# Optimization experiments

Hardware: AMD Instinct MI355X
Metric: run time of the kernel (lower is better)

Reference implementation:

```python
import jax, jax.numpy as jnp
import numpy as np

ALPHA = 0.2  # LeakyReLU negative slope
NEG_BIG = -9e15


def setup_inputs() -> dict:
    key = jax.random.key(0)
    k1, k2, k3, k4 = jax.random.split(key, 4)
    B, N, F_in, F_out = 8, 2048, 256, 256
    x = jax.random.normal(k1, (B, N, F_in), dtype=jnp.float32)
    adj = jax.random.randint(k2, (B, N, N), 0, 2, dtype=jnp.int32)
    # Xavier-uniform init like nn.init.xavier_uniform_
    limW = float(np.sqrt(6.0 / (F_in + F_out)))
    W = jax.random.uniform(k3, (F_in, F_out), minval=-limW, maxval=limW, dtype=jnp.float32)
    lima = float(np.sqrt(6.0 / (2 * F_out + 1)))
    a = jax.random.uniform(k4, (2 * F_out, 1), minval=-lima, maxval=lima, dtype=jnp.float32)
    return {"x": x, "adj": adj, "W": W, "a": a}


def reference(x, adj, W, a):
    # x: (B,N,Fin), adj: (B,N,N), W: (Fin,Fout), a: (2*Fout,1)
    F_out = W.shape[1]
    Wh = jnp.einsum('bnf,fo->bno', x, W)            # (B,N,Fout)
    a1, a2 = a[:F_out, 0], a[F_out:, 0]
    # e[b,i,j] = leakyrelu(Wh[b,i]@a1 + Wh[b,j]@a2)  (equivalent to concat+matmul)
    e = (Wh @ a1)[:, :, None] + (Wh @ a2)[:, None, :]  # (B,N,N)
    e = jnp.where(e > 0, e, ALPHA * e)
    attention = jnp.where(adj > 0, e, NEG_BIG)
    attention = jax.nn.softmax(attention, axis=-1)
    # dropout is identity in eval mode (training=False)
    h_prime = jnp.einsum('bij,bjo->bio', attention, Wh)  # (B,N,Fout)
    return jax.nn.elu(h_prime)  # concat=True -> ELU
```

## Files before the change

kernel.cpp:

```cpp
#include <hip/hip_runtime.h>
#include <hip/hip_fp16.h>

typedef _Float16 f16;
typedef _Float16 half4 __attribute__((ext_vector_type(4)));
typedef _Float16 half8 __attribute__((ext_vector_type(8)));
typedef float f32x4 __attribute__((ext_vector_type(4)));

#define BATCH 8
#define NTOK 2048
#define FIN 256
#define FOUT 256
#define ALPHA 0.2f


__device__ __forceinline__ void gload16(const void* g, void* l) {
    __builtin_amdgcn_global_load_lds(
        (const __attribute__((address_space(1))) unsigned int*)(g),
        (__attribute__((address_space(3))) unsigned int*)(l), 16, 0, 0);
}

__global__ void k_wt(const float* __restrict__ W, f16* __restrict__ WT) {
    __shared__ float t[32][33];
    int o0 = blockIdx.x * 32, k0 = blockIdx.y * 32;
    int tx = threadIdx.x, ty = threadIdx.y;
    t[ty][tx] = W[(k0 + ty) * FOUT + o0 + tx];
    __syncthreads();
    WT[(o0 + ty) * FIN + (k0 + tx)] = (f16)t[tx][ty];
}

__global__ __launch_bounds__(256) void k_gemm(const float* __restrict__ x,
                                              const f16* __restrict__ WT,
                                              const float* __restrict__ a,
                                              f16* __restrict__ WhT,
                                              float* __restrict__ s1,
                                              float* __restrict__ s2) {
    __shared__ __align__(16) char gsmem[46080];
    int t = threadIdx.x;
    int lane = t & 63, w = t >> 6;
    f16* Ah = (f16*)gsmem;
    f16* Bt = (f16*)(gsmem + 9216);
    int m0 = blockIdx.x * 64;
    int lr = lane & 15, lg = lane >> 4;
    f32x4 acc[4][4] = {};

    for (int k0 = 0; k0 < FIN; k0 += 64) {
        {
            int r = t >> 2, c = (t & 3) * 16;
            const float* src = x + (size_t)(m0 + r) * FIN + k0 + c;
            f32x4 v0 = *(const f32x4*)(src);
            f32x4 v1 = *(const f32x4*)(src + 4);
            f32x4 v2 = *(const f32x4*)(src + 8);
            f32x4 v3 = *(const f32x4*)(src + 12);
            half8 h0, h1;
#pragma unroll
            for (int q = 0; q < 4; q++) {
                h0[q] = (f16)v0[q]; h0[q + 4] = (f16)v1[q];
                h1[q] = (f16)v2[q]; h1[q + 4] = (f16)v3[q];
            }
            f16* dst = Ah + r * 72 + c;
            *(half8*)dst = h0;
            *(half8*)(dst + 8) = h1;
        }
        {
            const f16* src = WT + (size_t)t * FIN + k0;
            f16* dst = Bt + t * 72;
#pragma unroll
            for (int q = 0; q < 8; q++)
                *(half8*)(dst + q * 8) = *(const half8*)(src + q * 8);
        }
        __syncthreads();
#pragma unroll
        for (int kc = 0; kc < 2; kc++) {
            int krow = kc * 32 + lg * 8;
            half8 af[4], bf[4];
#pragma unroll
            for (int fi = 0; fi < 4; fi++)
                af[fi] = *(half8*)(Ah + (fi * 16 + lr) * 72 + krow);
#pragma unroll
            for (int fo = 0; fo < 4; fo++)
                bf[fo] = *(half8*)(Bt + (w * 64 + fo * 16 + lr) * 72 + krow);
#pragma unroll
            for (int fi = 0; fi < 4; fi++)
#pragma unroll
                for (int fo = 0; fo < 4; fo++)
                    acc[fi][fo] = __builtin_amdgcn_mfma_f32_16x16x32_f16(
                        af[fi], bf[fo], acc[fi][fo], 0, 0, 0);
        }
        __syncthreads();
    }

    int b = m0 >> 11;
    int slab_i = (m0 & (NTOK - 1)) >> 6;
    int nbase = m0 & (NTOK - 1);

    float* sred = (float*)gsmem;
    f16* slab = (f16*)(gsmem + 9216);
    float a1v[4], a2v[4];
#pragma unroll
    for (int fo = 0; fo < 4; fo++) {
        int o = w * 64 + fo * 16 + lr;
        a1v[fo] = a[o];
        a2v[fo] = a[FOUT + o];
    }
#pragma unroll
    for (int fi = 0; fi < 4; fi++) {
        f32x4 p1 = {}, p2 = {};
#pragma unroll
        for (int fo = 0; fo < 4; fo++) {
            p1 += acc[fi][fo] * a1v[fo];
            p2 += acc[fi][fo] * a2v[fo];
        }
#pragma unroll
        for (int q = 0; q < 4; q++) {
#pragma unroll
            for (int d = 1; d < 16; d <<= 1) {
                p1[q] += __shfl_xor(p1[q], d);
                p2[q] += __shfl_xor(p2[q], d);
            }
        }
        if (lr == 0) {
            int row = fi * 16 + lg * 4;
#pragma unroll
            for (int q = 0; q < 4; q++) {
                sred[w * 64 + row + q] = p1[q];
                sred[256 + w * 64 + row + q] = p2[q];
            }
        }
    }
#pragma unroll
    for (int fi = 0; fi < 4; fi++) {
        int jg8 = fi * 2 + (lg >> 1), jq0 = (lg & 1) * 4;
#pragma unroll
        for (int fo = 0; fo < 4; fo++) {
            int o = w * 64 + fo * 16 + lr;
            half4 hv;
#pragma unroll
            for (int q = 0; q < 4; q++) hv[q] = (f16)acc[fi][fo][q];
            *(half4*)(slab + o * 64 + ((jg8 ^ (o & 7)) * 8) + jq0) = hv;
        }
    }
    __syncthreads();

    if (t < 64) {
        s1[(size_t)b * NTOK + nbase + t] =
            sred[t] + sred[64 + t] + sred[128 + t] + sred[192 + t];
    } else if (t < 128) {
        int r2 = t - 64;
        s2[(size_t)b * NTOK + nbase + r2] =
            sred[256 + r2] + sred[320 + r2] + sred[384 + r2] + sred[448 + r2];
    }
    {
        const int4* sl = (const int4*)slab;
        int4* gd = (int4*)(WhT + ((size_t)(b * 32 + slab_i) * 256) * 64);
#pragma unroll
        for (int i = 0; i < 8; i++) gd[i * 256 + t] = sl[i * 256 + t];
    }
}

__global__ __launch_bounds__(512, 1) void k_attn(const int* __restrict__ adj,
                                                 const f16* __restrict__ WhT,
                                                 const float* __restrict__ s1g,
                                                 const float* __restrict__ s2g,
                                                 float* __restrict__ out) {
    __shared__ __align__(16) char smem[91264];
    f16* Bl = (f16*)smem;
    float* s2_lds = (float*)(smem + 65536);
    unsigned* mask_lds = (unsigned*)(smem + 73728);
    float* lpart = (float*)(smem + 90624);
    float* wmax = (float*)(smem + 91136);

    int b = blockIdx.x & 7;
    int i0 = (blockIdx.x >> 3) * 64;
    int t = threadIdx.x;
    int lane = t & 63, w = t >> 6;
    int js = w & 1, oh = (w >> 1) & 1, rg = w >> 2;
    int lr = lane & 15, lg = lane >> 4;

    {
        f32x4 sv4 = ((const f32x4*)(s2g + (size_t)b * NTOK))[t];
        ((f32x4*)s2_lds)[t] = sv4;
        float tmx = fmaxf(fmaxf(sv4[0], sv4[1]), fmaxf(sv4[2], sv4[3]));
#pragma unroll
        for (int d = 1; d < 64; d <<= 1) tmx = fmaxf(tmx, __shfl_xor(tmx, d));
        if (lane == 0) wmax[w] = tmx;
    }

    const char* wsrc = (const char*)WhT + (size_t)b * (32 * 32768);
    {
        const char* src = wsrc + (w * 4) * 1024 + lane * 16;
        char* dst = (char*)Bl + (w * 4) * 1024;
#pragma unroll
        for (int k = 0; k < 4; k++) gload16(src + k * 1024, dst + k * 1024);
    }

    {
        const int4* abase = (const int4*)(adj + ((size_t)(b * NTOK + i0 + w * 8)) * NTOK)
                            + lane * 8;
        int4 cur[8], nxt[8];
#pragma unroll
        for (int k = 0; k < 8; k++) cur[k] = abase[k];
        for (int r = 0; r < 8; r++) {
            if (r < 7) {
#pragma unroll
                for (int k = 0; k < 8; k++) nxt[k] = abase[(r + 1) * 512 + k];
            }
            unsigned m = 0;
#pragma unroll
            for (int k = 0; k < 8; k++) {
                m |= (unsigned)(cur[k].x > 0) << (k * 4);
                m |= (unsigned)(cur[k].y > 0) << (k * 4 + 1);
                m |= (unsigned)(cur[k].z > 0) << (k * 4 + 2);
                m |= (unsigned)(cur[k].w > 0) << (k * 4 + 3);
            }
            mask_lds[(w * 8 + r) * 66 + lane] = m;
#pragma unroll
            for (int k = 0; k < 8; k++) cur[k] = nxt[k];
        }
    }

    int rr0 = rg * 32 + lr;
    int r0 = i0 + rr0, r1 = r0 + 16;
    float s1r0 = s1g[(size_t)b * NTOK + r0];
    float s1r1 = s1g[(size_t)b * NTOK + r1];

    f32x4 acc0[8] = {}, acc1[8] = {};
    float l0 = 0.f, l1 = 0.f;
    int rswz = ((js * 4 + lg) ^ (lr & 7)) * 8;

    __syncthreads();

    float s2m = wmax[0];
#pragma unroll
    for (int k = 1; k < 8; k++) s2m = fmaxf(s2m, wmax[k]);
    float tx0 = s1r0 + s2m;
    float mx0 = fmaxf(tx0, ALPHA * tx0);
    float tx1 = s1r1 + s2m;
    float mx1 = fmaxf(tx1, ALPHA * tx1);

    for (int s = 0; s < 32; s++) {
        int buf = s & 1;
        if (s < 31) {
            const char* src = wsrc + (size_t)(s + 1) * 32768 + (w * 4) * 1024 + lane * 16;
            char* dst = (char*)Bl + (buf ^ 1) * 32768 + (w * 4) * 1024;
#pragma unroll
            for (int k = 0; k < 4; k++) gload16(src + k * 1024, dst + k * 1024);
        }

        unsigned cw0 = mask_lds[rr0 * 66 + s * 2 + js];
        unsigned cw1 = mask_lds[(rr0 + 16) * 66 + s * 2 + js];
        unsigned bits0 = (cw0 >> (lg * 8)) & 0xffu;
        unsigned bits1 = (cw1 >> (lg * 8)) & 0xffu;

        int sb = s * 64 + js * 32 + lg * 8;
        f32x4 sA = *(const f32x4*)&s2_lds[sb];
        f32x4 sB = *(const f32x4*)&s2_lds[sb + 4];

        half8 ph0, ph1;
#pragma unroll
        for (int q = 0; q < 8; q++) {
            float sv = q < 4 ? sA[q & 3] : sB[q & 3];
            float sx = s1r0 + sv;
            float ev = fmaxf(sx, ALPHA * sx);
            float p = ((bits0 >> q) & 1) ? __expf(ev - mx0) : 0.f;
            l0 += p; ph0[q] = (f16)p;
            float sy = s1r1 + sv;
            float eu = fmaxf(sy, ALPHA * sy);
            float u = ((bits1 >> q) & 1) ? __expf(eu - mx1) : 0.f;
            l1 += u; ph1[q] = (f16)u;
        }

        const f16* bbase = Bl + buf * 16384 + (oh * 128 + lr) * 64 + rswz;
#pragma unroll
        for (int ot = 0; ot < 8; ot++) {
            half8 bf = *(const half8*)(bbase + ot * (16 * 64));
            acc0[ot] = __builtin_amdgcn_mfma_f32_16x16x32_f16(ph0, bf, acc0[ot], 0, 0, 0);
            acc1[ot] = __builtin_amdgcn_mfma_f32_16x16x32_f16(ph1, bf, acc1[ot], 0, 0, 0);
        }
        __syncthreads();
    }

    l0 += __shfl_xor(l0, 16); l0 += __shfl_xor(l0, 32);
    l1 += __shfl_xor(l1, 16); l1 += __shfl_xor(l1, 32);
    if (oh == 0 && lg == 0) {
        lpart[js * 64 + rg * 32 + lr] = l0;
        lpart[js * 64 + rg * 32 + 16 + lr] = l1;
    }
    __syncthreads();

    float* accx = (float*)smem;
    if (js == 1) {
#pragma unroll
        for (int ot = 0; ot < 8; ot++)
#pragma unroll
            for (int q = 0; q < 4; q++) {
                accx[(rg * 32 + lg * 4 + q) * 260 + oh * 128 + ot * 16 + lr] = acc0[ot][q];
                accx[(rg * 32 + 16 + lg * 4 + q) * 260 + oh * 128 + ot * 16 + lr] = acc1[ot][q];
            }
    }
    __syncthreads();
    if (js == 0) {
        f32x4 rl0, rl1;
#pragma unroll
        for (int q = 0; q < 4; q++) {
            int ra = rg * 32 + lg * 4 + q, rb = ra + 16;
            rl0[q] = 1.f / (lpart[ra] + lpart[64 + ra]);
            rl1[q] = 1.f / (lpart[rb] + lpart[64 + rb]);
        }
#pragma unroll
        for (int ot = 0; ot < 8; ot++) {
            int o = oh * 128 + ot * 16 + lr;
#pragma unroll
            for (int q = 0; q < 4; q++) {
                int ra = rg * 32 + lg * 4 + q;
                float u = (acc0[ot][q] + accx[ra * 260 + o]) * rl0[q];
                u = u > 0.f ? u : __expf(u) - 1.f;
                __builtin_nontemporal_store(u, &out[((size_t)(b * NTOK + i0 + ra)) * FOUT + o]);
                int rb = ra + 16;
                float v = (acc1[ot][q] + accx[rb * 260 + o]) * rl1[q];
                v = v > 0.f ? v : __expf(v) - 1.f;
                __builtin_nontemporal_store(v, &out[((size_t)(b * NTOK + i0 + rb)) * FOUT + o]);
            }
        }
    }
}

extern "C" void kernel_launch(void* const* d_in, const int* in_sizes, int n_in,
                              void* d_out, int out_size, void* d_ws, size_t ws_size,
                              hipStream_t stream) {
    const float* x = (const float*)d_in[0];
    const int* adj = (const int*)d_in[1];
    const float* W = (const float*)d_in[2];
    const float* a = (const float*)d_in[3];
    float* out = (float*)d_out;

    char* ws = (char*)d_ws;
    f16* WT = (f16*)ws;
    f16* WhT = (f16*)(ws + 131072);
    float* s1 = (float*)(ws + 131072 + 8388608);
    float* s2 = s1 + BATCH * NTOK;

    k_wt<<<dim3(FOUT / 32, FIN / 32), dim3(32, 32), 0, stream>>>(W, WT);
    k_gemm<<<dim3(BATCH * NTOK / 64), 256, 0, stream>>>(x, WT, a, WhT, s1, s2);
    k_attn<<<dim3(BATCH * NTOK / 64), 512, 0, stream>>>(adj, WhT, s1, s2, out);
}
```

Baseline: 82.85 us.

## Compute softmax probabilities once into LDS and split MFMA work by output columns

Before, each warp pair split the key dimension, so every warp recomputed exp for 32 rows across half the keys, and the two halves were reduced through LDS at the end. Now each thread computes the probabilities for one row and eight keys exactly once per step and writes them as f16 into a swizzled LDS tile. All warps then read A fragments from that tile and each covers a quarter of the output columns, which removes the redundant exp work and the final cross-warp reduction. The change also folds log2e into s1/s2 so exp2f can be used, and issues the WhT prefetch two stages ahead. The cost is a second barrier per step, extra LDS traffic for P, and a larger LDS footprint.

```diff
diff --git a/kernel.cpp b/kernel.cpp
--- a/kernel.cpp
+++ b/kernel.cpp
@@ -11,6 +11,7 @@
 #define FIN 256
 #define FOUT 256
 #define ALPHA 0.2f
+#define LOG2E 1.44269504088896340736f
 
 
 __device__ __forceinline__ void gload16(const void* g, void* l) {
@@ -162,22 +163,26 @@
                                                  const float* __restrict__ s1g,
                                                  const float* __restrict__ s2g,
                                                  float* __restrict__ out) {
-    __shared__ __align__(16) char smem[91264];
+    __shared__ __align__(16) char smem[107296];
     f16* Bl = (f16*)smem;
     float* s2_lds = (float*)(smem + 65536);
     unsigned* mask_lds = (unsigned*)(smem + 73728);
-    float* lpart = (float*)(smem + 90624);
-    float* wmax = (float*)(smem + 91136);
+    f16* P_lds = (f16*)(smem + 90624);
+    float* l_lds = (float*)(smem + 107008);
+    float* wmax = (float*)(smem + 107264);
 
     int b = blockIdx.x & 7;
     int i0 = (blockIdx.x >> 3) * 64;
     int t = threadIdx.x;
     int lane = t & 63, w = t >> 6;
-    int js = w & 1, oh = (w >> 1) & 1, rg = w >> 2;
     int lr = lane & 15, lg = lane >> 4;
+    int oq = w & 3, rg = w >> 2;
+    int r4 = lane >> 3, j8 = lane & 7;
+    int srow = w * 8 + r4;
 
     {
         f32x4 sv4 = ((const f32x4*)(s2g + (size_t)b * NTOK))[t];
+        sv4 = sv4 * LOG2E;
         ((f32x4*)s2_lds)[t] = sv4;
         float tmx = fmaxf(fmaxf(sv4[0], sv4[1]), fmaxf(sv4[2], sv4[3]));
 #pragma unroll
@@ -187,139 +192,141 @@
 
     const char* wsrc = (const char*)WhT + (size_t)b * (32 * 32768);
     {
-        const char* src = wsrc + (w * 4) * 1024 + lane * 16;
-        char* dst = (char*)Bl + (w * 4) * 1024;
-#pragma unroll
-        for (int k = 0; k < 4; k++) gload16(src + k * 1024, dst + k * 1024);
+        const char* s0 = wsrc + w * 4096 + lane * 16;
+        char* d0 = (char*)Bl + w * 4096;
+#pragma unroll
+        for (int k = 0; k < 4; k++) gload16(s0 + k * 1024, d0 + k * 1024);
+        const char* s1p = wsrc + 32768 + w * 4096 + lane * 16;
+        char* d1 = (char*)Bl + 32768 + w * 4096;
+#pragma unroll
+        for (int k = 0; k < 4; k++) gload16(s1p + k * 1024, d1 + k * 1024);
     }
 
     {
         const int4* abase = (const int4*)(adj + ((size_t)(b * NTOK + i0 + w * 8)) * NTOK)
                             + lane * 8;
-        int4 cur[8], nxt[8];
-#pragma unroll
-        for (int k = 0; k < 8; k++) cur[k] = abase[k];
-        for (int r = 0; r < 8; r++) {
-            if (r < 7) {
-#pragma unroll
-                for (int k = 0; k < 8; k++) nxt[k] = abase[(r + 1) * 512 + k];
-            }
-            unsigned m = 0;
+        int4 c0[8], c1[8];
+#pragma unroll
+        for (int k = 0; k < 8; k++) { c0[k] = abase[k]; c1[k] = abase[512 + k]; }
+        for (int rp = 0; rp < 4; rp++) {
+            int4 n0[8], n1[8];
+            if (rp < 3) {
+#pragma unroll
+                for (int k = 0; k < 8; k++) {
+                    n0[k] = abase[(2 * rp + 2) * 512 + k];
+                    n1[k] = abase[(2 * rp + 3) * 512 + k];
+                }
+            }
+            unsigned m0 = 0, m1 = 0;
 #pragma unroll
             for (int k = 0; k < 8; k++) {
-                m |= (unsigned)(cur[k].x > 0) << (k * 4);
-                m |= (unsigned)(cur[k].y > 0) << (k * 4 + 1);
-                m |= (unsigned)(cur[k].z > 0) << (k * 4 + 2);
-                m |= (unsigned)(cur[k].w > 0) << (k * 4 + 3);
-            }
-            mask_lds[(w * 8 + r) * 66 + lane] = m;
-#pragma unroll
-            for (int k = 0; k < 8; k++) cur[k] = nxt[k];
-        }
-    }
-
-    int rr0 = rg * 32 + lr;
-    int r0 = i0 + rr0, r1 = r0 + 16;
-    float s1r0 = s1g[(size_t)b * NTOK + r0];
-    float s1r1 = s1g[(size_t)b * NTOK + r1];
-
-    f32x4 acc0[8] = {}, acc1[8] = {};
-    float l0 = 0.f, l1 = 0.f;
-    int rswz = ((js * 4 + lg) ^ (lr & 7)) * 8;
+                m0 |= (unsigned)(c0[k].x > 0) << (k * 4);
+                m0 |= (unsigned)(c0[k].y > 0) << (k * 4 + 1);
+                m0 |= (unsigned)(c0[k].z > 0) << (k * 4 + 2);
+                m0 |= (unsigned)(c0[k].w > 0) << (k * 4 + 3);
+                m1 |= (unsigned)(c1[k].x > 0) << (k * 4);
+                m1 |= (unsigned)(c1[k].y > 0) << (k * 4 + 1);
+                m1 |= (unsigned)(c1[k].z > 0) << (k * 4 + 2);
+                m1 |= (unsigned)(c1[k].w > 0) << (k * 4 + 3);
+            }
+            mask_lds[(w * 8 + 2 * rp) * 66 + lane] = m0;
+            mask_lds[(w * 8 + 2 * rp + 1) * 66 + lane] = m1;
+#pragma unroll
+            for (int k = 0; k < 8; k++) { c0[k] = n0[k]; c1[k] = n1[k]; }
+        }
+    }
+
+    float s1r = s1g[(size_t)b * NTOK + i0 + srow] * LOG2E;
+    float l_acc = 0.f;
 
     __syncthreads();
 
     float s2m = wmax[0];
 #pragma unroll
     for (int k = 1; k < 8; k++) s2m = fmaxf(s2m, wmax[k]);
-    float tx0 = s1r0 + s2m;
-    float mx0 = fmaxf(tx0, ALPHA * tx0);
-    float tx1 = s1r1 + s2m;
-    float mx1 = fmaxf(tx1, ALPHA * tx1);
+    float txr = s1r + s2m;
+    float mxr = fmaxf(txr, ALPHA * txr);
+
+    f32x4 acc[2][4] = {};
 
     for (int s = 0; s < 32; s++) {
         int buf = s & 1;
-        if (s < 31) {
-            const char* src = wsrc + (size_t)(s + 1) * 32768 + (w * 4) * 1024 + lane * 16;
-            char* dst = (char*)Bl + (buf ^ 1) * 32768 + (w * 4) * 1024;
+        {
+            unsigned mw = mask_lds[srow * 66 + s * 2 + (j8 >> 2)];
+            unsigned bits = (mw >> ((j8 & 3) * 8)) & 0xffu;
+            f32x4 sA = *(const f32x4*)&s2_lds[s * 64 + j8 * 8];
+            f32x4 sB = *(const f32x4*)&s2_lds[s * 64 + j8 * 8 + 4];
+            half8 ph;
+#pragma unroll
+            for (int q = 0; q < 8; q++) {
+                float sv = q < 4 ? sA[q] : sB[q - 4];
+                float sx = s1r + sv;
+                float ev = fmaxf(sx, ALPHA * sx);
+                float p = ((bits >> q) & 1) ? exp2f(ev - mxr) : 0.f;
+                l_acc += p;
+                ph[q] = (f16)p;
+            }
+            *(half8*)&P_lds[buf * 4096 + srow * 64 + ((j8 ^ (srow & 7)) * 8)] = ph;
+        }
+        __syncthreads();
+
+        {
+            const f16* Pb = P_lds + buf * 4096;
+            const f16* Bb = Bl + buf * 16384;
+            half8 af[2][2];
+#pragma unroll
+            for (int fi = 0; fi < 2; fi++)
+#pragma unroll
+                for (int kc = 0; kc < 2; kc++) {
+                    int ra = rg * 32 + fi * 16 + lr;
+                    af[fi][kc] = *(const half8*)&Pb[ra * 64 + (((kc * 4 + lg) ^ (ra & 7)) * 8)];
+                }
+#pragma unroll
+            for (int ot = 0; ot < 4; ot++) {
+                int o = oq * 64 + ot * 16 + lr;
+#pragma unroll
+                for (int kc = 0; kc < 2; kc++) {
+                    half8 bf = *(const half8*)&Bb[o * 64 + (((kc * 4 + lg) ^ (o & 7)) * 8)];
+                    acc[0][ot] = __builtin_amdgcn_mfma_f32_16x16x32_f16(af[0][kc], bf, acc[0][ot], 0, 0, 0);
+                    acc[1][ot] = __builtin_amdgcn_mfma_f32_16x16x32_f16(af[1][kc], bf, acc[1][ot], 0, 0, 0);
+                }
+            }
+        }
+        __syncthreads();
+
+        if (s < 30) {
+            const char* src = wsrc + (size_t)(s + 2) * 32768 + w * 4096 + lane * 16;
+            char* dst = (char*)Bl + buf * 32768 + w * 4096;
 #pragma unroll
             for (int k = 0; k < 4; k++) gload16(src + k * 1024, dst + k * 1024);
         }
-
-        unsigned cw0 = mask_lds[rr0 * 66 + s * 2 + js];
-        unsigned cw1 = mask_lds[(rr0 + 16) * 66 + s * 2 + js];
-        unsigned bits0 = (cw0 >> (lg * 8)) & 0xffu;
-        unsigned bits1 = (cw1 >> (lg * 8)) & 0xffu;
-
-        int sb = s * 64 + js * 32 + lg * 8;
-        f32x4 sA = *(const f32x4*)&s2_lds[sb];
-        f32x4 sB = *(const f32x4*)&s2_lds[sb + 4];
-
-        half8 ph0, ph1;
-#pragma unroll
-        for (int q = 0; q < 8; q++) {
-            float sv = q < 4 ? sA[q & 3] : sB[q & 3];
-            float sx = s1r0 + sv;
-            float ev = fmaxf(sx, ALPHA * sx);
-            float p = ((bits0 >> q) & 1) ? __expf(ev - mx0) : 0.f;
-            l0 += p; ph0[q] = (f16)p;
-            float sy = s1r1 + sv;
-            float eu = fmaxf(sy, ALPHA * sy);
-            float u = ((bits1 >> q) & 1) ? __expf(eu - mx1) : 0.f;
-            l1 += u; ph1[q] = (f16)u;
-        }
-
-        const f16* bbase = Bl + buf * 16384 + (oh * 128 + lr) * 64 + rswz;
-#pragma unroll
-        for (int ot = 0; ot < 8; ot++) {
-            half8 bf = *(const half8*)(bbase + ot * (16 * 64));
-            acc0[ot] = __builtin_amdgcn_mfma_f32_16x16x32_f16(ph0, bf, acc0[ot], 0, 0, 0);
-            acc1[ot] = __builtin_amdgcn_mfma_f32_16x16x32_f16(ph1, bf, acc1[ot], 0, 0, 0);
-        }
-        __syncthreads();
-    }
-
-    l0 += __shfl_xor(l0, 16); l0 += __shfl_xor(l0, 32);
-    l1 += __shfl_xor(l1, 16); l1 += __shfl_xor(l1, 32);
-    if (oh == 0 && lg == 0) {
-        lpart[js * 64 + rg * 32 + lr] = l0;
-        lpart[js * 64 + rg * 32 + 16 + lr] = l1;
-    }
+    }
+
+    l_acc += __shfl_xor(l_acc, 1);
+    l_acc += __shfl_xor(l_acc, 2);
+    l_acc += __shfl_xor(l_acc, 4);
+    if (j8 == 0) l_lds[srow] = l_acc;
     __syncthreads();
 
-    float* accx = (float*)smem;
-    if (js == 1) {
-#pragma unroll
-        for (int ot = 0; ot < 8; ot++)
-#pragma unroll
-            for (int q = 0; q < 4; q++) {
-                accx[(rg * 32 + lg * 4 + q) * 260 + oh * 128 + ot * 16 + lr] = acc0[ot][q];
-                accx[(rg * 32 + 16 + lg * 4 + q) * 260 + oh * 128 + ot * 16 + lr] = acc1[ot][q];
-            }
-    }
-    __syncthreads();
-    if (js == 0) {
-        f32x4 rl0, rl1;
+    f32x4 rl0, rl1;
+#pragma unroll
+    for (int q = 0; q < 4; q++) {
+        rl0[q] = 1.f / l_lds[rg * 32 + lg * 4 + q];
+        rl1[q] = 1.f / l_lds[rg * 32 + 16 + lg * 4 + q];
+    }
+#pragma unroll
+    for (int ot = 0; ot < 4; ot++) {
+        int o = oq * 64 + ot * 16 + lr;
 #pragma unroll
         for (int q = 0; q < 4; q++) {
-            int ra = rg * 32 + lg * 4 + q, rb = ra + 16;
-            rl0[q] = 1.f / (lpart[ra] + lpart[64 + ra]);
-            rl1[q] = 1.f / (lpart[rb] + lpart[64 + rb]);
-        }
-#pragma unroll
-        for (int ot = 0; ot < 8; ot++) {
-            int o = oh * 128 + ot * 16 + lr;
-#pragma unroll
-            for (int q = 0; q < 4; q++) {
-                int ra = rg * 32 + lg * 4 + q;
-                float u = (acc0[ot][q] + accx[ra * 260 + o]) * rl0[q];
-                u = u > 0.f ? u : __expf(u) - 1.f;
-                __builtin_nontemporal_store(u, &out[((size_t)(b * NTOK + i0 + ra)) * FOUT + o]);
-                int rb = ra + 16;
-                float v = (acc1[ot][q] + accx[rb * 260 + o]) * rl1[q];
-                v = v > 0.f ? v : __expf(v) - 1.f;
-                __builtin_nontemporal_store(v, &out[((size_t)(b * NTOK + i0 + rb)) * FOUT + o]);
-            }
+            int ra = rg * 32 + lg * 4 + q;
+            float u = acc[0][ot][q] * rl0[q];
+            u = u > 0.f ? u : __expf(u) - 1.f;
+            __builtin_nontemporal_store(u, &out[((size_t)(b * NTOK + i0 + ra)) * FOUT + o]);
+            int rb = ra + 16;
+            float v = acc[1][ot][q] * rl1[q];
+            v = v > 0.f ? v : __expf(v) - 1.f;
+            __builtin_nontemporal_store(v, &out[((size_t)(b * NTOK + i0 + rb)) * FOUT + o]);
         }
     }
 }
```

Result: no change. 83.05 us (+0.2%).
